# Performance work log

Hardware: AMD Instinct MI355X
Metric: run time of the kernel (lower is better)

Reference implementation:

```python
import jax, jax.numpy as jnp
import numpy as np
import math

B, S, H = 8, 4096, 1024
E, I, K = 8, 2048, 2
CAP_FACTOR = 1.0


def setup_inputs() -> dict:
    key = jax.random.key(0)
    k1, k2, k3, k4 = jax.random.split(key, 4)
    # kaiming_uniform (linear): bound = sqrt(3 / fan_in), fan_in = last dim
    def kaiming(k, shape):
        bound = math.sqrt(3.0 / shape[-1])
        return jax.random.uniform(k, shape, jnp.float32, -bound, bound)
    x = jax.random.normal(k1, (B, S, H), jnp.float32)
    expert_embeddings = kaiming(k2, (E, H))
    first_linear = kaiming(k3, (E, I, H))
    second_linear = kaiming(k4, (E, H, I))
    return {"x": x, "expert_embeddings": expert_embeddings,
            "first_linear": first_linear, "second_linear": second_linear}


def _router(x, expert_embeddings):
    # dot: [B, S, E]
    dot = jnp.einsum('bsh,eh->bse', x, expert_embeddings)
    n = dot.shape[0] * dot.shape[1]
    dot2 = dot.reshape(n, E)
    vals, idx = jax.lax.top_k(dot2, K)                       # [N, K]
    rows = jnp.arange(n)[:, None]
    masked = jnp.full_like(dot2, -jnp.inf).at[rows, idx].set(vals)
    return jax.nn.softmax(masked, axis=-1)                   # [N, E]


def reference(x, expert_embeddings, first_linear, second_linear):
    batch, seq, hidden = x.shape
    n_tokens = batch * seq
    expert_capacity = math.ceil(n_tokens / E * CAP_FACTOR)

    weights = _router(x, expert_embeddings)                  # [N, E]
    ones = (weights > 0).astype(weights.dtype)               # tokens routed to expert
    # capacity mask: keep first expert_capacity tokens (in token order) per expert
    cap_ones = jnp.where(jnp.cumsum(ones, axis=0) <= expert_capacity, ones, 0.0)
    caw = weights * cap_ones                                 # [N, E]

    # topk over token dim per expert -> selected token slots
    vals, idx = jax.lax.top_k(caw.T, expert_capacity)        # [E, C]
    index = idx.reshape(-1)                                  # [E*C]

    x_flat = x.reshape(n_tokens, hidden)
    tokens = x_flat[index].reshape(E, expert_capacity, hidden)   # gather

    inter = jax.nn.relu(jnp.einsum('ech,eih->eci', tokens, first_linear))
    out = jnp.einsum('eci,ehi->ech', inter, second_linear)
    out = out * vals[:, :, None]                             # weight by router prob

    final = jnp.zeros((n_tokens, hidden), x.dtype).at[index].add(
        out.reshape(-1, hidden))                             # scatter-add combine
    return final.reshape(x.shape)
```

## Files before the change

### kernel.cpp

```cpp
#include <hip/hip_runtime.h>
#include <stdint.h>

#define N_TOK 32768
#define HID   1024
#define NE    8
#define NI    2048
#define CAP   4096

typedef short s16x8 __attribute__((ext_vector_type(8)));
typedef float f32x4 __attribute__((ext_vector_type(4)));

__device__ __forceinline__ unsigned short f2bf(float f) {
    unsigned int u = __builtin_bit_cast(unsigned int, f);
    u += 0x7fffu + ((u >> 16) & 1u);
    return (unsigned short)(u >> 16);
}

__device__ __forceinline__ void gload16(const void* g, void* l) {
    __builtin_amdgcn_global_load_lds(
        (const __attribute__((address_space(1))) unsigned int*)(uintptr_t)g,
        (__attribute__((address_space(3))) unsigned int*)(unsigned int)(uintptr_t)l,
        16, 0, 0);
}

__global__ __launch_bounds__(256) void cvt2_kernel(
    const float* __restrict__ s1, unsigned short* __restrict__ d1, size_t n81,
    const float* __restrict__ s2, unsigned short* __restrict__ d2, size_t n82)
{
    size_t i = (size_t)blockIdx.x * 256 + threadIdx.x;
    size_t stride = (size_t)gridDim.x * 256;
    size_t total = n81 + n82;
    for (; i < total; i += stride) {
        const float* src; unsigned short* dst; size_t j;
        if (i < n81) { src = s1; dst = d1; j = i; }
        else         { src = s2; dst = d2; j = i - n81; }
        float4 a0 = ((const float4*)src)[2 * j];
        float4 a1 = ((const float4*)src)[2 * j + 1];
        uint4 p;
        p.x = f2bf(a0.x) | ((unsigned)f2bf(a0.y) << 16);
        p.y = f2bf(a0.z) | ((unsigned)f2bf(a0.w) << 16);
        p.z = f2bf(a1.x) | ((unsigned)f2bf(a1.y) << 16);
        p.w = f2bf(a1.z) | ((unsigned)f2bf(a1.w) << 16);
        ((uint4*)dst)[j] = p;
    }
}

__global__ __launch_bounds__(256) void router_kernel(
    const float* __restrict__ x, const float* __restrict__ emb,
    int2* __restrict__ r_e, float2* __restrict__ r_w,
    unsigned short* __restrict__ xb)
{
    int token = blockIdx.x * 4 + (threadIdx.x >> 6);
    int lane  = threadIdx.x & 63;
    const float4* xr = (const float4*)(x + (size_t)token * HID);
    const float4* er = (const float4*)emb;

    float a[NE];
#pragma unroll
    for (int e = 0; e < NE; ++e) a[e] = 0.f;
    uint2 pk[4];
#pragma unroll
    for (int j = 0; j < 4; ++j) {
        float4 v = xr[j * 64 + lane];
        pk[j].x = f2bf(v.x) | ((unsigned)f2bf(v.y) << 16);
        pk[j].y = f2bf(v.z) | ((unsigned)f2bf(v.w) << 16);
#pragma unroll
        for (int e = 0; e < NE; ++e) {
            float4 w = er[e * 256 + j * 64 + lane];
            a[e] += v.x * w.x + v.y * w.y + v.z * w.z + v.w * w.w;
        }
    }
    uint2* xbr = (uint2*)(xb + (size_t)token * HID);
#pragma unroll
    for (int j = 0; j < 4; ++j) xbr[j * 64 + lane] = pk[j];

#pragma unroll
    for (int e = 0; e < NE; ++e) {
        for (int off = 32; off; off >>= 1) a[e] += __shfl_xor(a[e], off);
    }
    if (lane == 0) {
        float v1 = -1e30f, v2 = -1e30f; int i1 = 0, i2 = 0;
#pragma unroll
        for (int e = 0; e < NE; ++e) {
            float v = a[e];
            if (v > v1) { v2 = v1; i2 = i1; v1 = v; i1 = e; }
            else if (v > v2) { v2 = v; i2 = e; }
        }
        float ex = __expf(v2 - v1);
        r_e[token] = make_int2(i1, i2);
        r_w[token] = make_float2(1.f / (1.f + ex), ex / (1.f + ex));
    }
}

__global__ __launch_bounds__(1024) void count_kernel(
    const int2* __restrict__ r_e, int* __restrict__ bc)
{
    __shared__ int cnt[NE];
    if (threadIdx.x < NE) cnt[threadIdx.x] = 0;
    __syncthreads();
    int n = blockIdx.x * 1024 + threadIdx.x;
    int2 e = r_e[n];
    atomicAdd(&cnt[e.x], 1);
    atomicAdd(&cnt[e.y], 1);
    __syncthreads();
    if (threadIdx.x < NE) bc[blockIdx.x * NE + threadIdx.x] = cnt[threadIdx.x];
}

__global__ void prefix_kernel(const int* __restrict__ bc, int* __restrict__ bb)
{
    int e = threadIdx.x;
    if (e >= NE) return;
    int run = 0;
    for (int b = 0; b < N_TOK / 1024; ++b) {
        bb[b * NE + e] = run;
        run += bc[b * NE + e];
    }
}

__global__ __launch_bounds__(1024) void assign_kernel(
    const int2* __restrict__ r_e, const float2* __restrict__ r_w,
    const int* __restrict__ bb,
    int* __restrict__ tok_list, float* __restrict__ w_list)
{
    __shared__ int wavecnt[16][NE];
    __shared__ int waveoff[16][NE];
    int tid = threadIdx.x, lane = tid & 63, wv = tid >> 6;
    int n = blockIdx.x * 1024 + tid;
    int2 e = r_e[n];
    float2 w = r_w[n];
    unsigned long long below = (1ull << lane) - 1ull;
    int rank0 = 0, rank1 = 0;
#pragma unroll
    for (int ex = 0; ex < NE; ++ex) {
        unsigned long long m = __ballot(e.x == ex || e.y == ex);
        if (lane == 0) wavecnt[wv][ex] = __popcll(m);
        int r = __popcll(m & below);
        if (e.x == ex) rank0 = r;
        if (e.y == ex) rank1 = r;
    }
    __syncthreads();
    if (tid < NE) {
        int run = 0;
        for (int w2 = 0; w2 < 16; ++w2) { waveoff[w2][tid] = run; run += wavecnt[w2][tid]; }
    }
    __syncthreads();
    int s0 = bb[blockIdx.x * NE + e.x] + waveoff[wv][e.x] + rank0;
    int s1 = bb[blockIdx.x * NE + e.y] + waveoff[wv][e.y] + rank1;
    if (s0 < CAP) { tok_list[e.x * CAP + s0] = n; w_list[e.x * CAP + s0] = w.x; }
    if (s1 < CAP) { tok_list[e.y * CAP + s1] = n; w_list[e.y * CAP + s1] = w.y; }
}


__global__ __launch_bounds__(256, 4) void gemm1_k(
    const unsigned short* __restrict__ xb,
    const unsigned short* __restrict__ w1b,
    const int* __restrict__ tok_list,
    unsigned short* __restrict__ inter,
    int eb)
{
    constexpr int K = HID, T = K / 64;
    __shared__ __align__(16) unsigned short smem[16384];
    unsigned short* As = smem;
    unsigned short* Bs = smem + 8192;

    const int nblk = gridDim.x;
    const int lin  = blockIdx.x;
    const int wg   = (lin & 7) * (nblk >> 3) + (lin >> 3);
    const int tn = wg & 15;
    const int tm = (wg >> 4) & 31;
    const int ez = wg >> 9;
    const int e  = eb + ez;

    const int tid = threadIdx.x, lane = tid & 63, wave = tid >> 6;
    const int wr = wave >> 1, wc = wave & 1;
    const int gsl8 = ((lane & 7) ^ ((lane >> 3) & 7)) * 8;
    const int abase = (wr * 64 + (lane & 15)) * 64;
    const int bbase = (wc * 64 + (lane & 15)) * 64;
    const int phs[2] = { (((lane >> 4)) ^ (lane & 7)) * 8,
                         ((4 + (lane >> 4)) ^ (lane & 7)) * 8 };

    const int* tl = tok_list + e * CAP + tm * 128;
    const unsigned short* srcA[4];
    const unsigned short* srcB[4];
#pragma unroll
    for (int c = 0; c < 4; ++c) {
        int row = c * 32 + wave * 8 + (lane >> 3);
        srcA[c] = xb + (size_t)tl[row] * K + gsl8;
        srcB[c] = w1b + ((size_t)e * NI + tn * 128 + row) * K + gsl8;
    }

    f32x4 acc[4][4];
#pragma unroll
    for (int i = 0; i < 4; ++i)
#pragma unroll
        for (int j = 0; j < 4; ++j) acc[i][j] = (f32x4)0.f;

    for (int t = 0; t < T; ++t) {
#pragma unroll
        for (int c = 0; c < 4; ++c) {
            unsigned short* d = smem + (c * 32 + wave * 8) * 64;
            gload16(srcA[c] + t * 64, d);
            gload16(srcB[c] + t * 64, d + 8192);
        }
        __syncthreads();
#pragma unroll
        for (int ks = 0; ks < 2; ++ks) {
            s16x8 af[4], bf[4];
#pragma unroll
            for (int mi = 0; mi < 4; ++mi)
                af[mi] = *(const s16x8*)(As + abase + mi * 1024 + phs[ks]);
#pragma unroll
            for (int ni = 0; ni < 4; ++ni)
                bf[ni] = *(const s16x8*)(Bs + bbase + ni * 1024 + phs[ks]);
#pragma unroll
            for (int mi = 0; mi < 4; ++mi)
#pragma unroll
                for (int ni = 0; ni < 4; ++ni)
                    acc[mi][ni] = __builtin_amdgcn_mfma_f32_16x16x32_bf16(
                        af[mi], bf[ni], acc[mi][ni], 0, 0, 0);
        }
        __syncthreads();
    }

#pragma unroll
    for (int mi = 0; mi < 4; ++mi)
#pragma unroll
        for (int ni = 0; ni < 4; ++ni)
#pragma unroll
            for (int r = 0; r < 4; ++r) {
                int row = wr * 64 + mi * 16 + (lane >> 4) * 4 + r;
                int c   = wc * 64 + ni * 16 + (lane & 15);
                float v = acc[mi][ni][r];
                v = v > 0.f ? v : 0.f;
                smem[row * 128 + (((c >> 3) ^ (row & 7)) << 3) + (c & 7)] = f2bf(v);
            }
    __syncthreads();
    unsigned short* Cp = inter + ((size_t)ez * CAP + tm * 128) * NI + tn * 128;
#pragma unroll
    for (int it = 0; it < 8; ++it) {
        int v = tid + it * 256;
        int row = v >> 4, s = v & 15;
        uint4 val = *(const uint4*)&smem[row * 128 + ((s ^ (row & 7)) << 3)];
        *(uint4*)&Cp[(size_t)row * NI + s * 8] = val;
    }
}

__global__ __launch_bounds__(256, 4) void gemm2_k(
    const unsigned short* __restrict__ inter,
    const unsigned short* __restrict__ w2b,
    const int* __restrict__ tok_list,
    const float* __restrict__ w_list,
    float* __restrict__ out,
    int eb)
{
    constexpr int K = NI, T = K / 64;
    __shared__ __align__(16) unsigned short smem[16384];
    unsigned short* As = smem;
    unsigned short* Bs = smem + 8192;

    const int nblk = gridDim.x;
    const int lin  = blockIdx.x;
    const int wg   = (lin & 7) * (nblk >> 3) + (lin >> 3);
    const int tn = wg & 7;
    const int tm = (wg >> 3) & 31;
    const int ez = wg >> 8;
    const int e  = eb + ez;

    const int tid = threadIdx.x, lane = tid & 63, wave = tid >> 6;
    const int wr = wave >> 1, wc = wave & 1;
    const int gsl8 = ((lane & 7) ^ ((lane >> 3) & 7)) * 8;
    const int abase = (wr * 64 + (lane & 15)) * 64;
    const int bbase = (wc * 64 + (lane & 15)) * 64;
    const int phs[2] = { (((lane >> 4)) ^ (lane & 7)) * 8,
                         ((4 + (lane >> 4)) ^ (lane & 7)) * 8 };

    const unsigned short* srcA[4];
    const unsigned short* srcB[4];
#pragma unroll
    for (int c = 0; c < 4; ++c) {
        int row = c * 32 + wave * 8 + (lane >> 3);
        srcA[c] = inter + ((size_t)ez * CAP + tm * 128 + row) * (size_t)K + gsl8;
        srcB[c] = w2b + ((size_t)e * HID + tn * 128 + row) * (size_t)K + gsl8;
    }

    f32x4 acc[4][4];
#pragma unroll
    for (int i = 0; i < 4; ++i)
#pragma unroll
        for (int j = 0; j < 4; ++j) acc[i][j] = (f32x4)0.f;

    for (int t = 0; t < T; ++t) {
#pragma unroll
        for (int c = 0; c < 4; ++c) {
            unsigned short* d = smem + (c * 32 + wave * 8) * 64;
            gload16(srcA[c] + t * 64, d);
            gload16(srcB[c] + t * 64, d + 8192);
        }
        __syncthreads();
#pragma unroll
        for (int ks = 0; ks < 2; ++ks) {
            s16x8 af[4], bf[4];
#pragma unroll
            for (int mi = 0; mi < 4; ++mi)
                af[mi] = *(const s16x8*)(As + abase + mi * 1024 + phs[ks]);
#pragma unroll
            for (int ni = 0; ni < 4; ++ni)
                bf[ni] = *(const s16x8*)(Bs + bbase + ni * 1024 + phs[ks]);
#pragma unroll
            for (int mi = 0; mi < 4; ++mi)
#pragma unroll
                for (int ni = 0; ni < 4; ++ni)
                    acc[mi][ni] = __builtin_amdgcn_mfma_f32_16x16x32_bf16(
                        af[mi], bf[ni], acc[mi][ni], 0, 0, 0);
        }
        __syncthreads();
    }

    const int* tl   = tok_list + e * CAP + tm * 128;
    const float* wl = w_list  + e * CAP + tm * 128;
#pragma unroll
    for (int mi = 0; mi < 4; ++mi)
#pragma unroll
        for (int r = 0; r < 4; ++r) {
            int rrow = wr * 64 + mi * 16 + (lane >> 4) * 4 + r;
            int tok  = tl[rrow];
            float w  = wl[rrow];
            float* orow = out + (size_t)tok * HID + tn * 128 + wc * 64;
#pragma unroll
            for (int ni = 0; ni < 4; ++ni)
                atomicAdd(&orow[ni * 16 + (lane & 15)], acc[mi][ni][r] * w);
        }
}

extern "C" void kernel_launch(void* const* d_in, const int* in_sizes, int n_in,
                              void* d_out, int out_size, void* d_ws, size_t ws_size,
                              hipStream_t stream)
{
    const float* x   = (const float*)d_in[0];
    const float* emb = (const float*)d_in[1];
    const float* W1  = (const float*)d_in[2];
    const float* W2  = (const float*)d_in[3];
    float* out = (float*)d_out;

    size_t off = 0;
    auto alloc = [&](size_t bytes) -> void* {
        void* p = (char*)d_ws + off;
        off += (bytes + 255) & ~(size_t)255;
        return p;
    };
    const size_t sz_w  = (size_t)NE * NI * HID * 2;
    const size_t sz_xb = (size_t)N_TOK * HID * 2;

    int*   tok_list = (int*)alloc((size_t)NE * CAP * 4);
    float* w_list   = (float*)alloc((size_t)NE * CAP * 4);
    unsigned short* w1b = (unsigned short*)alloc(sz_w);
    unsigned short* w2b = (unsigned short*)alloc(sz_w);
    unsigned short* xb  = (unsigned short*)alloc(sz_xb);

    unsigned short* inter = (unsigned short*)((char*)d_ws + off);
    size_t avail = ws_size > off ? ws_size - off : 0;
    const size_t per_e = (size_t)CAP * NI * 2;
    int G = (avail >= 8 * per_e) ? 8 : (avail >= 4 * per_e) ? 4
          : (avail >= 2 * per_e) ? 2 : 1;

    int2*   r_e = (int2*)inter;
    float2* r_w = (float2*)((char*)inter + (size_t)N_TOK * 8);
    int*    bc  = (int*)((char*)inter + (size_t)N_TOK * 16);
    int*    bb  = bc + (N_TOK / 1024) * NE;

    hipMemsetAsync(d_out, 0, (size_t)N_TOK * HID * 4, stream);
    hipMemsetAsync(tok_list, 0, (size_t)NE * CAP * 4, stream);
    hipMemsetAsync(w_list, 0, (size_t)NE * CAP * 4, stream);

    cvt2_kernel<<<2048, 256, 0, stream>>>(W1, w1b, (size_t)NE * NI * HID / 8,
                                          W2, w2b, (size_t)NE * HID * NI / 8);
    router_kernel<<<N_TOK / 4, 256, 0, stream>>>(x, emb, r_e, r_w, xb);
    count_kernel<<<N_TOK / 1024, 1024, 0, stream>>>(r_e, bc);
    prefix_kernel<<<1, 64, 0, stream>>>(bc, bb);
    assign_kernel<<<N_TOK / 1024, 1024, 0, stream>>>(r_e, r_w, bb, tok_list, w_list);

    for (int eb = 0; eb < NE; eb += G) {
        gemm1_k<<<dim3(16 * 32 * G), 256, 0, stream>>>(xb, w1b, tok_list, inter, eb);
        gemm2_k<<<dim3(8 * 32 * G), 256, 0, stream>>>(inter, w2b, tok_list, w_list, out, eb);
    }
}
```

Baseline: 463.6 us.

## Replace atomic scatter-add with bf16 expert output buffer and gather combine

When all experts fit in workspace, gemm2 writes its un-weighted expert outputs as bf16 through a swizzled LDS staging tile into a per-slot buffer that reuses the xb region, instead of doing fp32 atomicAdds into the output. A new combine kernel reads each token's two slots through a token-to-slot map written by assign_kernel, weights them and writes the output directly, so the output memset is dropped. This removes atomic traffic and the zero-fill pass, but adds an extra kernel, an intermediate round-trip through memory and a bf16 rounding of the expert outputs.

```diff
diff --git a/kernel.cpp b/kernel.cpp
--- a/kernel.cpp
+++ b/kernel.cpp
@@ -14,6 +14,10 @@
     unsigned int u = __builtin_bit_cast(unsigned int, f);
     u += 0x7fffu + ((u >> 16) & 1u);
     return (unsigned short)(u >> 16);
+}
+
+__device__ __forceinline__ float bf2f(unsigned short u) {
+    return __builtin_bit_cast(float, (unsigned int)u << 16);
 }
 
 __device__ __forceinline__ void gload16(const void* g, void* l) {
@@ -120,7 +124,8 @@
 __global__ __launch_bounds__(1024) void assign_kernel(
     const int2* __restrict__ r_e, const float2* __restrict__ r_w,
     const int* __restrict__ bb,
-    int* __restrict__ tok_list, float* __restrict__ w_list)
+    int* __restrict__ tok_list, float* __restrict__ w_list,
+    int2* __restrict__ smap)
 {
     __shared__ int wavecnt[16][NE];
     __shared__ int waveoff[16][NE];
@@ -146,8 +151,41 @@
     __syncthreads();
     int s0 = bb[blockIdx.x * NE + e.x] + waveoff[wv][e.x] + rank0;
     int s1 = bb[blockIdx.x * NE + e.y] + waveoff[wv][e.y] + rank1;
-    if (s0 < CAP) { tok_list[e.x * CAP + s0] = n; w_list[e.x * CAP + s0] = w.x; }
-    if (s1 < CAP) { tok_list[e.y * CAP + s1] = n; w_list[e.y * CAP + s1] = w.y; }
+    int g0 = -1, g1 = -1;
+    if (s0 < CAP) { tok_list[e.x * CAP + s0] = n; w_list[e.x * CAP + s0] = w.x; g0 = e.x * CAP + s0; }
+    if (s1 < CAP) { tok_list[e.y * CAP + s1] = n; w_list[e.y * CAP + s1] = w.y; g1 = e.y * CAP + s1; }
+    smap[n] = make_int2(g0, g1);
+}
+
+__global__ __launch_bounds__(256) void combine_kernel(
+    const unsigned short* __restrict__ out_e,
+    const int2* __restrict__ smap,
+    const float* __restrict__ w_list,
+    float* __restrict__ out)
+{
+    int t  = blockIdx.x * 2 + (threadIdx.x >> 7);
+    int h0 = (threadIdx.x & 127) * 8;
+    int2 s = smap[t];
+    float r[8];
+#pragma unroll
+    for (int i = 0; i < 8; ++i) r[i] = 0.f;
+    if (s.x >= 0) {
+        float w = w_list[s.x];
+        uint4 v = *(const uint4*)(out_e + (size_t)s.x * HID + h0);
+        const unsigned short* pv = (const unsigned short*)&v;
+#pragma unroll
+        for (int i = 0; i < 8; ++i) r[i] += w * bf2f(pv[i]);
+    }
+    if (s.y >= 0) {
+        float w = w_list[s.y];
+        uint4 v = *(const uint4*)(out_e + (size_t)s.y * HID + h0);
+        const unsigned short* pv = (const unsigned short*)&v;
+#pragma unroll
+        for (int i = 0; i < 8; ++i) r[i] += w * bf2f(pv[i]);
+    }
+    float4* o = (float4*)(out + (size_t)t * HID + h0);
+    o[0] = make_float4(r[0], r[1], r[2], r[3]);
+    o[1] = make_float4(r[4], r[5], r[6], r[7]);
 }
 
 
@@ -251,6 +289,7 @@
     const int* __restrict__ tok_list,
     const float* __restrict__ w_list,
     float* __restrict__ out,
+    unsigned short* __restrict__ out_e,
     int eb)
 {
     constexpr int K = NI, T = K / 64;
@@ -316,20 +355,42 @@
         __syncthreads();
     }
 
-    const int* tl   = tok_list + e * CAP + tm * 128;
-    const float* wl = w_list  + e * CAP + tm * 128;
-#pragma unroll
-    for (int mi = 0; mi < 4; ++mi)
-#pragma unroll
-        for (int r = 0; r < 4; ++r) {
-            int rrow = wr * 64 + mi * 16 + (lane >> 4) * 4 + r;
-            int tok  = tl[rrow];
-            float w  = wl[rrow];
-            float* orow = out + (size_t)tok * HID + tn * 128 + wc * 64;
+    if (out_e) {
+#pragma unroll
+        for (int mi = 0; mi < 4; ++mi)
 #pragma unroll
             for (int ni = 0; ni < 4; ++ni)
-                atomicAdd(&orow[ni * 16 + (lane & 15)], acc[mi][ni][r] * w);
-        }
+#pragma unroll
+                for (int r = 0; r < 4; ++r) {
+                    int row = wr * 64 + mi * 16 + (lane >> 4) * 4 + r;
+                    int c   = wc * 64 + ni * 16 + (lane & 15);
+                    smem[row * 128 + (((c >> 3) ^ (row & 7)) << 3) + (c & 7)] = f2bf(acc[mi][ni][r]);
+                }
+        __syncthreads();
+        unsigned short* Cp = out_e + ((size_t)e * CAP + tm * 128) * HID + tn * 128;
+#pragma unroll
+        for (int it = 0; it < 8; ++it) {
+            int v = tid + it * 256;
+            int row = v >> 4, s = v & 15;
+            uint4 val = *(const uint4*)&smem[row * 128 + ((s ^ (row & 7)) << 3)];
+            *(uint4*)&Cp[(size_t)row * HID + s * 8] = val;
+        }
+    } else {
+        const int* tl   = tok_list + e * CAP + tm * 128;
+        const float* wl = w_list  + e * CAP + tm * 128;
+#pragma unroll
+        for (int mi = 0; mi < 4; ++mi)
+#pragma unroll
+            for (int r = 0; r < 4; ++r) {
+                int rrow = wr * 64 + mi * 16 + (lane >> 4) * 4 + r;
+                int tok  = tl[rrow];
+                float w  = wl[rrow];
+                float* orow = out + (size_t)tok * HID + tn * 128 + wc * 64;
+#pragma unroll
+                for (int ni = 0; ni < 4; ++ni)
+                    atomicAdd(&orow[ni * 16 + (lane & 15)], acc[mi][ni][r] * w);
+            }
+    }
 }
 
 extern "C" void kernel_launch(void* const* d_in, const int* in_sizes, int n_in,
@@ -353,6 +414,7 @@
 
     int*   tok_list = (int*)alloc((size_t)NE * CAP * 4);
     float* w_list   = (float*)alloc((size_t)NE * CAP * 4);
+    int2*  smap     = (int2*)alloc((size_t)N_TOK * 8);
     unsigned short* w1b = (unsigned short*)alloc(sz_w);
     unsigned short* w2b = (unsigned short*)alloc(sz_w);
     unsigned short* xb  = (unsigned short*)alloc(sz_xb);
@@ -362,13 +424,16 @@
     const size_t per_e = (size_t)CAP * NI * 2;
     int G = (avail >= 8 * per_e) ? 8 : (avail >= 4 * per_e) ? 4
           : (avail >= 2 * per_e) ? 2 : 1;
+    const bool combine = (G == 8);
+    unsigned short* out_e = combine ? xb : nullptr;
 
     int2*   r_e = (int2*)inter;
     float2* r_w = (float2*)((char*)inter + (size_t)N_TOK * 8);
     int*    bc  = (int*)((char*)inter + (size_t)N_TOK * 16);
     int*    bb  = bc + (N_TOK / 1024) * NE;
 
-    hipMemsetAsync(d_out, 0, (size_t)N_TOK * HID * 4, stream);
+    if (!combine)
+        hipMemsetAsync(d_out, 0, (size_t)N_TOK * HID * 4, stream);
     hipMemsetAsync(tok_list, 0, (size_t)NE * CAP * 4, stream);
     hipMemsetAsync(w_list, 0, (size_t)NE * CAP * 4, stream);
 
@@ -377,10 +442,12 @@
     router_kernel<<<N_TOK / 4, 256, 0, stream>>>(x, emb, r_e, r_w, xb);
     count_kernel<<<N_TOK / 1024, 1024, 0, stream>>>(r_e, bc);
     prefix_kernel<<<1, 64, 0, stream>>>(bc, bb);
-    assign_kernel<<<N_TOK / 1024, 1024, 0, stream>>>(r_e, r_w, bb, tok_list, w_list);
+    assign_kernel<<<N_TOK / 1024, 1024, 0, stream>>>(r_e, r_w, bb, tok_list, w_list, smap);
 
     for (int eb = 0; eb < NE; eb += G) {
         gemm1_k<<<dim3(16 * 32 * G), 256, 0, stream>>>(xb, w1b, tok_list, inter, eb);
-        gemm2_k<<<dim3(8 * 32 * G), 256, 0, stream>>>(inter, w2b, tok_list, w_list, out, eb);
-    }
-}
+        gemm2_k<<<dim3(8 * 32 * G), 256, 0, stream>>>(inter, w2b, tok_list, w_list, out, out_e, eb);
+    }
+    if (combine)
+        combine_kernel<<<N_TOK / 2, 256, 0, stream>>>(out_e, smap, w_list, out);
+}
```

Result: faster. 420.8 us (median of 2 runs) (-9.2%).
